# Kernel optimization log

Measured on AMD Instinct MI355X. Metric: run time of the kernel, lower is better.

## Reference

```python
import jax, jax.numpy as jnp
import numpy as np

H = 181  # hidden size

def setup_inputs() -> dict:
    key = jax.random.key(0)
    ks = jax.random.split(key, 7)
    B, T, I, C = 1024, 1024, 1, 10
    x = jax.random.normal(ks[0], (B, T, I), dtype=jnp.float32)
    w_ih = jax.random.normal(ks[1], (3 * H, I), dtype=jnp.float32) * 0.5
    w_hh = jax.random.normal(ks[2], (3 * H, H), dtype=jnp.float32) * (1.0 / np.sqrt(H))
    b_ih = jax.random.normal(ks[3], (3 * H,), dtype=jnp.float32) * 0.1
    b_hh = jax.random.normal(ks[4], (3 * H,), dtype=jnp.float32) * 0.1
    w_fc = jax.random.normal(ks[5], (C, H), dtype=jnp.float32) * (1.0 / np.sqrt(H))
    b_fc = jax.random.normal(ks[6], (C,), dtype=jnp.float32) * 0.1
    return {"x": x, "w_ih": w_ih, "w_hh": w_hh, "b_ih": b_ih, "b_hh": b_hh,
            "w_fc": w_fc, "b_fc": b_fc}

def _gru_last_hidden(x, w_ih, w_hh, b_ih, b_hh):
    # x: [B, T, I]. Precompute input-side gate pre-activations for all steps.
    B = x.shape[0]
    gi = jnp.einsum('bti,gi->btg', x, w_ih) + b_ih  # [B, T, 3H]
    gi = jnp.swapaxes(gi, 0, 1)                     # [T, B, 3H] for scan
    h0 = jnp.zeros((B, H), dtype=x.dtype)

    def step(h, gi_t):
        gh = h @ w_hh.T + b_hh                      # [B, 3H]
        r = jax.nn.sigmoid(gi_t[:, :H] + gh[:, :H])
        z = jax.nn.sigmoid(gi_t[:, H:2 * H] + gh[:, H:2 * H])
        n = jnp.tanh(gi_t[:, 2 * H:] + r * gh[:, 2 * H:])
        h_new = (1.0 - z) * n + z * h
        return h_new, None

    h_last, _ = jax.lax.scan(step, h0, gi)
    return h_last  # [B, H]

def reference(x, w_ih, w_hh, b_ih, b_hh, w_fc, b_fc):
    h_last = _gru_last_hidden(x, w_ih, w_hh, b_ih, b_hh)
    logits = h_last @ w_fc.T + b_fc  # [B, num_classes]
    return logits
```

## Files before the change

### kernel.cpp

```cpp
#include <hip/hip_runtime.h>

#define H 181
#define T_LEN 1024
#define BB 4
#define NBLK 256
#define NTHR 768
#define KT3 3
#define FRAGB 1024
#define PST 192
#define XSTR 1027

typedef __attribute__((ext_vector_type(4))) int intx4;

#define LOG2E 1.4426950408889634f
#define SCH_C  1064992506.0f
#define SCH_LO 897220352.0f
#define SCH_HI 1182433024.0f

__device__ __forceinline__ float exp2_fast(float g) {
    float s = fmaf(g, 8388608.0f, SCH_C);
    s = fminf(fmaxf(s, SCH_LO), SCH_HI);
    return __uint_as_float((unsigned)s);
}
__device__ __forceinline__ float rcpf(float x)   { return __builtin_amdgcn_rcpf(x); }
__device__ __forceinline__ float exp2hw(float x) { return __builtin_amdgcn_exp2f(x); }

__device__ __forceinline__ float row_scale(const float* wrow, bool mv) {
    float rm = 0.0f;
    if (mv) for (int k = 0; k < H; ++k) rm = fmaxf(rm, fabsf(wrow[k]));
    return (rm > 1e-30f) ? rm * (1.0f / 127.0f) : 1.0f;
}

__device__ __forceinline__ intx4 build_frag(const float* wrow, float invs,
                                            bool mv, int kt, int q) {
    intx4 frag;
    #pragma unroll
    for (int w = 0; w < 4; ++w) {
        int dw = 0;
        #pragma unroll
        for (int e = 0; e < 4; ++e) {
            int k = kt * 64 + q * 16 + w * 4 + e;
            float v = (mv && k < H) ? wrow[k] * invs : 0.0f;
            v = fminf(fmaxf(rintf(v), -127.0f), 127.0f);
            int iv = (int)v;
            dw |= (iv & 255) << (8 * e);
        }
        frag[w] = dw;
    }
    return frag;
}

__launch_bounds__(NTHR, 3)
__global__ void gru_i8(const float* __restrict__ x,
                       const float* __restrict__ w_ih,
                       const float* __restrict__ w_hh,
                       const float* __restrict__ b_ih,
                       const float* __restrict__ b_hh,
                       const float* __restrict__ w_fc,
                       const float* __restrict__ b_fc,
                       float* __restrict__ out) {
    __shared__ __align__(16) char  hfr_s[2 * KT3 * FRAGB];
    __shared__ __align__(16) float x_s[BB * XSTR];
    __shared__ float wsc_s[3 * PST];
    __shared__ volatile char pad_s[57344];

    const int tid  = threadIdx.x;
    const int jt   = tid >> 6;
    const int lane = tid & 63;
    const int col  = lane & 15;
    const int q    = lane >> 4;
    const int b0   = blockIdx.x * BB;
    if (tid == 0) pad_s[0] = 0;

    const int  mu = jt * 16 + col;
    const bool mv = (mu < H);
    const float* wrowR = w_hh + (size_t)(0 * H + (mv ? mu : 0)) * H;
    const float* wrowZ = w_hh + (size_t)(1 * H + (mv ? mu : 0)) * H;
    const float* wrowN = w_hh + (size_t)(2 * H + (mv ? mu : 0)) * H;
    const float sR = row_scale(wrowR, mv);
    const float sZ = row_scale(wrowZ, mv);
    const float sN = row_scale(wrowN, mv);
    const float iR = 1.0f / sR, iZ = 1.0f / sZ, iN = 1.0f / sN;
    const intx4 afR0 = build_frag(wrowR, iR, mv, 0, q);
    const intx4 afR1 = build_frag(wrowR, iR, mv, 1, q);
    const intx4 afR2 = build_frag(wrowR, iR, mv, 2, q);
    const intx4 afZ0 = build_frag(wrowZ, iZ, mv, 0, q);
    const intx4 afZ1 = build_frag(wrowZ, iZ, mv, 1, q);
    const intx4 afZ2 = build_frag(wrowZ, iZ, mv, 2, q);
    const intx4 afN0 = build_frag(wrowN, iN, mv, 0, q);
    const intx4 afN1 = build_frag(wrowN, iN, mv, 1, q);
    const intx4 afN2 = build_frag(wrowN, iN, mv, 2, q);
    if (q == 0) {
        wsc_s[0 * PST + mu] = sR;
        wsc_s[1 * PST + mu] = sZ;
        wsc_s[2 * PST + mu] = sN;
    }

    for (int i = tid; i < BB * T_LEN; i += NTHR) {
        int bb = i >> 10, t = i & 1023;
        x_s[bb * XSTR + t] = x[(size_t)b0 * T_LEN + i];
    }
    {
        int* hz = (int*)hfr_s;
        for (int i = tid; i < 2 * KT3 * FRAGB / 4; i += NTHR) hz[i] = 0;
    }
    __syncthreads();

    const int  rr4 = (col >> 2) & 3;
    const int  b   = col & 3;
    const int  u   = jt * 16 + q * 4 + rr4;
    const bool jv  = (u < H);
    const float dqR = -LOG2E * wsc_s[0 * PST + u] * (1.0f / 127.0f);
    const float dqZ = -LOG2E * wsc_s[1 * PST + u] * (1.0f / 127.0f);
    const float dqN =  2.0f * LOG2E * wsc_s[2 * PST + u] * (1.0f / 127.0f);
    const float baseR = jv ? -LOG2E * (b_ih[u] + b_hh[u])             : 0.0f;
    const float baseZ = jv ? -LOG2E * (b_ih[H + u] + b_hh[H + u])     : 0.0f;
    const float baseN = jv ?  2.0f * LOG2E * b_hh[2 * H + u]          : 0.0f;
    const float wrS = jv ? -LOG2E * w_ih[u]                : 0.0f;
    const float wzS = jv ? -LOG2E * w_ih[H + u]            : 0.0f;
    const float wnS = jv ?  2.0f * LOG2E * w_ih[2 * H + u] : 0.0f;
    const float bnI = jv ?  2.0f * LOG2E * b_ih[2 * H + u] : 0.0f;
    const int wboff8 = (jt >> 2) * FRAGB + (((jt & 3) * 16 + b) * 16) + q * 4 + rr4;
    const int rbase = lane * 16;

    float h = 0.0f;

#define STEP(rb, wb, t_) do {                                                 \
    intx4 bf0 = *(const intx4*)((rb) + 0 * FRAGB + rbase);                    \
    intx4 bf1 = *(const intx4*)((rb) + 1 * FRAGB + rbase);                    \
    intx4 bf2 = *(const intx4*)((rb) + 2 * FRAGB + rbase);                    \
    intx4 aR = {0,0,0,0}, aZ = {0,0,0,0}, aN = {0,0,0,0};                     \
    aR = __builtin_amdgcn_mfma_i32_16x16x64_i8(afR0, bf0, aR, 0, 0, 0);       \
    aZ = __builtin_amdgcn_mfma_i32_16x16x64_i8(afZ0, bf0, aZ, 0, 0, 0);       \
    aN = __builtin_amdgcn_mfma_i32_16x16x64_i8(afN0, bf0, aN, 0, 0, 0);       \
    aR = __builtin_amdgcn_mfma_i32_16x16x64_i8(afR1, bf1, aR, 0, 0, 0);       \
    aZ = __builtin_amdgcn_mfma_i32_16x16x64_i8(afZ1, bf1, aZ, 0, 0, 0);       \
    aN = __builtin_amdgcn_mfma_i32_16x16x64_i8(afN1, bf1, aN, 0, 0, 0);       \
    aR = __builtin_amdgcn_mfma_i32_16x16x64_i8(afR2, bf2, aR, 0, 0, 0);       \
    aZ = __builtin_amdgcn_mfma_i32_16x16x64_i8(afZ2, bf2, aZ, 0, 0, 0);       \
    aN = __builtin_amdgcn_mfma_i32_16x16x64_i8(afN2, bf2, aN, 0, 0, 0);       \
    int vR = aR[0], vZ = aZ[0], vN = aN[0];                                   \
    vR = __builtin_amdgcn_update_dpp(vR, aR[1], 0x114, 0xF, 0x2, false);      \
    vR = __builtin_amdgcn_update_dpp(vR, aR[2], 0x118, 0xF, 0x4, false);      \
    vR = __builtin_amdgcn_update_dpp(vR, aR[3], 0x11C, 0xF, 0x8, false);      \
    vZ = __builtin_amdgcn_update_dpp(vZ, aZ[1], 0x114, 0xF, 0x2, false);      \
    vZ = __builtin_amdgcn_update_dpp(vZ, aZ[2], 0x118, 0xF, 0x4, false);      \
    vZ = __builtin_amdgcn_update_dpp(vZ, aZ[3], 0x11C, 0xF, 0x8, false);      \
    vN = __builtin_amdgcn_update_dpp(vN, aN[1], 0x114, 0xF, 0x2, false);      \
    vN = __builtin_amdgcn_update_dpp(vN, aN[2], 0x118, 0xF, 0x4, false);      \
    vN = __builtin_amdgcn_update_dpp(vN, aN[3], 0x11C, 0xF, 0x8, false);      \
    float pR = fmaf((float)vR, dqR, baseR);                                   \
    float pZ = fmaf((float)vZ, dqZ, baseZ);                                   \
    float pN = fmaf((float)vN, dqN, baseN);                                   \
    float xv = x_s[b * XSTR + (t_)];                                          \
    float er = exp2_fast(fmaf(xv, wrS, pR));                                  \
    float ez = exp2hw(fminf(fmaf(xv, wzS, pZ), 14.0f));                       \
    float dR = 1.0f + er, dZ = 1.0f + ez;                                     \
    float qq = rcpf(dR * dZ);                                                 \
    float rr = qq * dZ, zz = qq * dR;                                         \
    float gn = fmaf(rr, pN, fmaf(xv, wnS, bnI));                              \
    float en = exp2hw(fminf(gn, 30.0f));                                      \
    float nn = fmaf(-2.0f, rcpf(1.0f + en), 1.0f);                            \
    h = fmaf(zz, h - nn, nn);                                                 \
    int hq = __float_as_int(fmaf(h, 127.0f, 12582912.0f));                    \
    *(char*)((wb) + wboff8) = (char)hq;                                       \
    __syncthreads();                                                          \
} while (0)

    char* buf0 = hfr_s;
    char* buf1 = hfr_s + KT3 * FRAGB;
    for (int t = 0; t < T_LEN; t += 2) {
        STEP(buf0, buf1, t);
        STEP(buf1, buf0, t + 1);
    }
#undef STEP

    __syncthreads();
    if (u < PST) x_s[b * PST + u] = h;
    __syncthreads();
    if (tid < BB * 10) {
        int bb = tid / 10, c = tid % 10;
        float acc = b_fc[c];
        for (int k = 0; k < H; ++k)
            acc = fmaf(x_s[bb * PST + k], w_fc[c * H + k], acc);
        out[(b0 + bb) * 10 + c] = acc;
    }
}

extern "C" void kernel_launch(void* const* d_in, const int* in_sizes, int n_in,
                              void* d_out, int out_size, void* d_ws, size_t ws_size,
                              hipStream_t stream) {
    const float* x    = (const float*)d_in[0];
    const float* w_ih = (const float*)d_in[1];
    const float* w_hh = (const float*)d_in[2];
    const float* b_ih = (const float*)d_in[3];
    const float* b_hh = (const float*)d_in[4];
    const float* w_fc = (const float*)d_in[5];
    const float* b_fc = (const float*)d_in[6];
    float* out = (float*)d_out;

    gru_i8<<<NBLK, NTHR, 0, stream>>>(x, w_ih, w_hh, b_ih, b_hh, w_fc, b_fc, out);
}
```

Measured before the change: 671.5 us.

## Cut block to 8 waves with first four waves owning two unit tiles

Shrinks each block from 12 to 8 wavefronts: waves 0-3 each handle two 16-unit tiles (A and B) while waves 4-7 handle one, so the 12 tiles of the hidden dimension are still covered. Fewer waves per block means cheaper per-step __syncthreads barriers and less scheduling overhead. In exchange, the critical path for the doubled waves roughly doubles the MFMA and gate work per step, register pressure rises from holding twice the weight fragments, and occupancy drops to two blocks per CU by launch bounds.

```diff
diff --git a/kernel.cpp b/kernel.cpp
--- a/kernel.cpp
+++ b/kernel.cpp
@@ -4,7 +4,7 @@
 #define T_LEN 1024
 #define BB 4
 #define NBLK 256
-#define NTHR 768
+#define NTHR 512
 #define KT3 3
 #define FRAGB 1024
 #define PST 192
@@ -50,7 +50,7 @@
     return frag;
 }
 
-__launch_bounds__(NTHR, 3)
+__launch_bounds__(NTHR, 2)
 __global__ void gru_i8(const float* __restrict__ x,
                        const float* __restrict__ w_ih,
                        const float* __restrict__ w_hh,
@@ -70,30 +70,58 @@
     const int col  = lane & 15;
     const int q    = lane >> 4;
     const int b0   = blockIdx.x * BB;
+    const bool two = (jt < 4);
     if (tid == 0) pad_s[0] = 0;
 
-    const int  mu = jt * 16 + col;
-    const bool mv = (mu < H);
-    const float* wrowR = w_hh + (size_t)(0 * H + (mv ? mu : 0)) * H;
-    const float* wrowZ = w_hh + (size_t)(1 * H + (mv ? mu : 0)) * H;
-    const float* wrowN = w_hh + (size_t)(2 * H + (mv ? mu : 0)) * H;
-    const float sR = row_scale(wrowR, mv);
-    const float sZ = row_scale(wrowZ, mv);
-    const float sN = row_scale(wrowN, mv);
-    const float iR = 1.0f / sR, iZ = 1.0f / sZ, iN = 1.0f / sN;
-    const intx4 afR0 = build_frag(wrowR, iR, mv, 0, q);
-    const intx4 afR1 = build_frag(wrowR, iR, mv, 1, q);
-    const intx4 afR2 = build_frag(wrowR, iR, mv, 2, q);
-    const intx4 afZ0 = build_frag(wrowZ, iZ, mv, 0, q);
-    const intx4 afZ1 = build_frag(wrowZ, iZ, mv, 1, q);
-    const intx4 afZ2 = build_frag(wrowZ, iZ, mv, 2, q);
-    const intx4 afN0 = build_frag(wrowN, iN, mv, 0, q);
-    const intx4 afN1 = build_frag(wrowN, iN, mv, 1, q);
-    const intx4 afN2 = build_frag(wrowN, iN, mv, 2, q);
+    const int  muA = jt * 16 + col;
+    const bool mvA = (muA < H);
+    const float* wrAR = w_hh + (size_t)(0 * H + (mvA ? muA : 0)) * H;
+    const float* wrAZ = w_hh + (size_t)(1 * H + (mvA ? muA : 0)) * H;
+    const float* wrAN = w_hh + (size_t)(2 * H + (mvA ? muA : 0)) * H;
+    const float sAR = row_scale(wrAR, mvA);
+    const float sAZ = row_scale(wrAZ, mvA);
+    const float sAN = row_scale(wrAN, mvA);
+    const intx4 aAR0 = build_frag(wrAR, 1.0f / sAR, mvA, 0, q);
+    const intx4 aAR1 = build_frag(wrAR, 1.0f / sAR, mvA, 1, q);
+    const intx4 aAR2 = build_frag(wrAR, 1.0f / sAR, mvA, 2, q);
+    const intx4 aAZ0 = build_frag(wrAZ, 1.0f / sAZ, mvA, 0, q);
+    const intx4 aAZ1 = build_frag(wrAZ, 1.0f / sAZ, mvA, 1, q);
+    const intx4 aAZ2 = build_frag(wrAZ, 1.0f / sAZ, mvA, 2, q);
+    const intx4 aAN0 = build_frag(wrAN, 1.0f / sAN, mvA, 0, q);
+    const intx4 aAN1 = build_frag(wrAN, 1.0f / sAN, mvA, 1, q);
+    const intx4 aAN2 = build_frag(wrAN, 1.0f / sAN, mvA, 2, q);
     if (q == 0) {
-        wsc_s[0 * PST + mu] = sR;
-        wsc_s[1 * PST + mu] = sZ;
-        wsc_s[2 * PST + mu] = sN;
+        wsc_s[0 * PST + muA] = sAR;
+        wsc_s[1 * PST + muA] = sAZ;
+        wsc_s[2 * PST + muA] = sAN;
+    }
+
+    const int  muB = (8 + jt) * 16 + col;
+    const bool mvB = two && (muB < H);
+    intx4 aBR0 = {0,0,0,0}, aBR1 = {0,0,0,0}, aBR2 = {0,0,0,0};
+    intx4 aBZ0 = {0,0,0,0}, aBZ1 = {0,0,0,0}, aBZ2 = {0,0,0,0};
+    intx4 aBN0 = {0,0,0,0}, aBN1 = {0,0,0,0}, aBN2 = {0,0,0,0};
+    if (two) {
+        const float* wrBR = w_hh + (size_t)(0 * H + (mvB ? muB : 0)) * H;
+        const float* wrBZ = w_hh + (size_t)(1 * H + (mvB ? muB : 0)) * H;
+        const float* wrBN = w_hh + (size_t)(2 * H + (mvB ? muB : 0)) * H;
+        const float sBR = row_scale(wrBR, mvB);
+        const float sBZ = row_scale(wrBZ, mvB);
+        const float sBN = row_scale(wrBN, mvB);
+        aBR0 = build_frag(wrBR, 1.0f / sBR, mvB, 0, q);
+        aBR1 = build_frag(wrBR, 1.0f / sBR, mvB, 1, q);
+        aBR2 = build_frag(wrBR, 1.0f / sBR, mvB, 2, q);
+        aBZ0 = build_frag(wrBZ, 1.0f / sBZ, mvB, 0, q);
+        aBZ1 = build_frag(wrBZ, 1.0f / sBZ, mvB, 1, q);
+        aBZ2 = build_frag(wrBZ, 1.0f / sBZ, mvB, 2, q);
+        aBN0 = build_frag(wrBN, 1.0f / sBN, mvB, 0, q);
+        aBN1 = build_frag(wrBN, 1.0f / sBN, mvB, 1, q);
+        aBN2 = build_frag(wrBN, 1.0f / sBN, mvB, 2, q);
+        if (q == 0) {
+            wsc_s[0 * PST + muB] = sBR;
+            wsc_s[1 * PST + muB] = sBZ;
+            wsc_s[2 * PST + muB] = sBN;
+        }
     }
 
     for (int i = tid; i < BB * T_LEN; i += NTHR) {
@@ -108,62 +136,101 @@
 
     const int  rr4 = (col >> 2) & 3;
     const int  b   = col & 3;
-    const int  u   = jt * 16 + q * 4 + rr4;
-    const bool jv  = (u < H);
-    const float dqR = -LOG2E * wsc_s[0 * PST + u] * (1.0f / 127.0f);
-    const float dqZ = -LOG2E * wsc_s[1 * PST + u] * (1.0f / 127.0f);
-    const float dqN =  2.0f * LOG2E * wsc_s[2 * PST + u] * (1.0f / 127.0f);
-    const float baseR = jv ? -LOG2E * (b_ih[u] + b_hh[u])             : 0.0f;
-    const float baseZ = jv ? -LOG2E * (b_ih[H + u] + b_hh[H + u])     : 0.0f;
-    const float baseN = jv ?  2.0f * LOG2E * b_hh[2 * H + u]          : 0.0f;
-    const float wrS = jv ? -LOG2E * w_ih[u]                : 0.0f;
-    const float wzS = jv ? -LOG2E * w_ih[H + u]            : 0.0f;
-    const float wnS = jv ?  2.0f * LOG2E * w_ih[2 * H + u] : 0.0f;
-    const float bnI = jv ?  2.0f * LOG2E * b_ih[2 * H + u] : 0.0f;
-    const int wboff8 = (jt >> 2) * FRAGB + (((jt & 3) * 16 + b) * 16) + q * 4 + rr4;
+    const int  uA  = jt * 16 + q * 4 + rr4;
+    const int  uB  = (8 + jt) * 16 + q * 4 + rr4;
+    const bool jvA = (uA < H);
+    const bool jvB = two && (uB < H);
+    const float dqRA = -LOG2E * wsc_s[0 * PST + uA] * (1.0f / 127.0f);
+    const float dqZA = -LOG2E * wsc_s[1 * PST + uA] * (1.0f / 127.0f);
+    const float dqNA =  2.0f * LOG2E * wsc_s[2 * PST + uA] * (1.0f / 127.0f);
+    const float baseRA = jvA ? -LOG2E * (b_ih[uA] + b_hh[uA])         : 0.0f;
+    const float baseZA = jvA ? -LOG2E * (b_ih[H + uA] + b_hh[H + uA]) : 0.0f;
+    const float baseNA = jvA ?  2.0f * LOG2E * b_hh[2 * H + uA]       : 0.0f;
+    const float wrSA = jvA ? -LOG2E * w_ih[uA]                : 0.0f;
+    const float wzSA = jvA ? -LOG2E * w_ih[H + uA]            : 0.0f;
+    const float wnSA = jvA ?  2.0f * LOG2E * w_ih[2 * H + uA] : 0.0f;
+    const float bnIA = jvA ?  2.0f * LOG2E * b_ih[2 * H + uA] : 0.0f;
+    const float dqRB = -LOG2E * wsc_s[0 * PST + uB] * (1.0f / 127.0f);
+    const float dqZB = -LOG2E * wsc_s[1 * PST + uB] * (1.0f / 127.0f);
+    const float dqNB =  2.0f * LOG2E * wsc_s[2 * PST + uB] * (1.0f / 127.0f);
+    const float baseRB = jvB ? -LOG2E * (b_ih[uB] + b_hh[uB])         : 0.0f;
+    const float baseZB = jvB ? -LOG2E * (b_ih[H + uB] + b_hh[H + uB]) : 0.0f;
+    const float baseNB = jvB ?  2.0f * LOG2E * b_hh[2 * H + uB]       : 0.0f;
+    const float wrSB = jvB ? -LOG2E * w_ih[uB]                : 0.0f;
+    const float wzSB = jvB ? -LOG2E * w_ih[H + uB]            : 0.0f;
+    const float wnSB = jvB ?  2.0f * LOG2E * w_ih[2 * H + uB] : 0.0f;
+    const float bnIB = jvB ?  2.0f * LOG2E * b_ih[2 * H + uB] : 0.0f;
+    const int woffA = (jt >> 2) * FRAGB + (((jt & 3) * 16 + b) * 16) + q * 4 + rr4;
+    const int woffB = ((8 + jt) >> 2) * FRAGB + ((((8 + jt) & 3) * 16 + b) * 16) + q * 4 + rr4;
     const int rbase = lane * 16;
 
-    float h = 0.0f;
+    float hA = 0.0f, hB = 0.0f;
+
+#define GATES(vR_, vZ_, vN_, dqR_, dqZ_, dqN_, baseR_, baseZ_, baseN_,       \
+              wrS_, wzS_, wnS_, bnI_, h_, wb, woff_) do {                     \
+    float pR = fmaf((float)(vR_), dqR_, baseR_);                              \
+    float pZ = fmaf((float)(vZ_), dqZ_, baseZ_);                              \
+    float pN = fmaf((float)(vN_), dqN_, baseN_);                              \
+    float er = exp2_fast(fmaf(xv, wrS_, pR));                                 \
+    float ez = exp2hw(fminf(fmaf(xv, wzS_, pZ), 14.0f));                      \
+    float dR = 1.0f + er, dZ = 1.0f + ez;                                     \
+    float qq = rcpf(dR * dZ);                                                 \
+    float rr = qq * dZ, zz = qq * dR;                                         \
+    float gn = fmaf(rr, pN, fmaf(xv, wnS_, bnI_));                            \
+    float en = exp2hw(fminf(gn, 30.0f));                                      \
+    float nn = fmaf(-2.0f, rcpf(1.0f + en), 1.0f);                            \
+    h_ = fmaf(zz, h_ - nn, nn);                                               \
+    int hq = __float_as_int(fmaf(h_, 127.0f, 12582912.0f));                   \
+    *(char*)((wb) + (woff_)) = (char)hq;                                      \
+} while (0)
+
+#define DPP3(v_, a_) do {                                                     \
+    v_ = a_[0];                                                               \
+    v_ = __builtin_amdgcn_update_dpp(v_, a_[1], 0x114, 0xF, 0x2, false);      \
+    v_ = __builtin_amdgcn_update_dpp(v_, a_[2], 0x118, 0xF, 0x4, false);      \
+    v_ = __builtin_amdgcn_update_dpp(v_, a_[3], 0x11C, 0xF, 0x8, false);      \
+} while (0)
 
 #define STEP(rb, wb, t_) do {                                                 \
     intx4 bf0 = *(const intx4*)((rb) + 0 * FRAGB + rbase);                    \
     intx4 bf1 = *(const intx4*)((rb) + 1 * FRAGB + rbase);                    \
     intx4 bf2 = *(const intx4*)((rb) + 2 * FRAGB + rbase);                    \
-    intx4 aR = {0,0,0,0}, aZ = {0,0,0,0}, aN = {0,0,0,0};                     \
-    aR = __builtin_amdgcn_mfma_i32_16x16x64_i8(afR0, bf0, aR, 0, 0, 0);       \
-    aZ = __builtin_amdgcn_mfma_i32_16x16x64_i8(afZ0, bf0, aZ, 0, 0, 0);       \
-    aN = __builtin_amdgcn_mfma_i32_16x16x64_i8(afN0, bf0, aN, 0, 0, 0);       \
-    aR = __builtin_amdgcn_mfma_i32_16x16x64_i8(afR1, bf1, aR, 0, 0, 0);       \
-    aZ = __builtin_amdgcn_mfma_i32_16x16x64_i8(afZ1, bf1, aZ, 0, 0, 0);       \
-    aN = __builtin_amdgcn_mfma_i32_16x16x64_i8(afN1, bf1, aN, 0, 0, 0);       \
-    aR = __builtin_amdgcn_mfma_i32_16x16x64_i8(afR2, bf2, aR, 0, 0, 0);       \
-    aZ = __builtin_amdgcn_mfma_i32_16x16x64_i8(afZ2, bf2, aZ, 0, 0, 0);       \
-    aN = __builtin_amdgcn_mfma_i32_16x16x64_i8(afN2, bf2, aN, 0, 0, 0);       \
-    int vR = aR[0], vZ = aZ[0], vN = aN[0];                                   \
-    vR = __builtin_amdgcn_update_dpp(vR, aR[1], 0x114, 0xF, 0x2, false);      \
-    vR = __builtin_amdgcn_update_dpp(vR, aR[2], 0x118, 0xF, 0x4, false);      \
-    vR = __builtin_amdgcn_update_dpp(vR, aR[3], 0x11C, 0xF, 0x8, false);      \
-    vZ = __builtin_amdgcn_update_dpp(vZ, aZ[1], 0x114, 0xF, 0x2, false);      \
-    vZ = __builtin_amdgcn_update_dpp(vZ, aZ[2], 0x118, 0xF, 0x4, false);      \
-    vZ = __builtin_amdgcn_update_dpp(vZ, aZ[3], 0x11C, 0xF, 0x8, false);      \
-    vN = __builtin_amdgcn_update_dpp(vN, aN[1], 0x114, 0xF, 0x2, false);      \
-    vN = __builtin_amdgcn_update_dpp(vN, aN[2], 0x118, 0xF, 0x4, false);      \
-    vN = __builtin_amdgcn_update_dpp(vN, aN[3], 0x11C, 0xF, 0x8, false);      \
-    float pR = fmaf((float)vR, dqR, baseR);                                   \
-    float pZ = fmaf((float)vZ, dqZ, baseZ);                                   \
-    float pN = fmaf((float)vN, dqN, baseN);                                   \
     float xv = x_s[b * XSTR + (t_)];                                          \
-    float er = exp2_fast(fmaf(xv, wrS, pR));                                  \
-    float ez = exp2hw(fminf(fmaf(xv, wzS, pZ), 14.0f));                       \
-    float dR = 1.0f + er, dZ = 1.0f + ez;                                     \
-    float qq = rcpf(dR * dZ);                                                 \
-    float rr = qq * dZ, zz = qq * dR;                                         \
-    float gn = fmaf(rr, pN, fmaf(xv, wnS, bnI));                              \
-    float en = exp2hw(fminf(gn, 30.0f));                                      \
-    float nn = fmaf(-2.0f, rcpf(1.0f + en), 1.0f);                            \
-    h = fmaf(zz, h - nn, nn);                                                 \
-    int hq = __float_as_int(fmaf(h, 127.0f, 12582912.0f));                    \
-    *(char*)((wb) + wboff8) = (char)hq;                                       \
+    intx4 cR = {0,0,0,0}, cZ = {0,0,0,0}, cN = {0,0,0,0};                     \
+    cR = __builtin_amdgcn_mfma_i32_16x16x64_i8(aAR0, bf0, cR, 0, 0, 0);       \
+    cZ = __builtin_amdgcn_mfma_i32_16x16x64_i8(aAZ0, bf0, cZ, 0, 0, 0);       \
+    cN = __builtin_amdgcn_mfma_i32_16x16x64_i8(aAN0, bf0, cN, 0, 0, 0);       \
+    cR = __builtin_amdgcn_mfma_i32_16x16x64_i8(aAR1, bf1, cR, 0, 0, 0);       \
+    cZ = __builtin_amdgcn_mfma_i32_16x16x64_i8(aAZ1, bf1, cZ, 0, 0, 0);       \
+    cN = __builtin_amdgcn_mfma_i32_16x16x64_i8(aAN1, bf1, cN, 0, 0, 0);       \
+    cR = __builtin_amdgcn_mfma_i32_16x16x64_i8(aAR2, bf2, cR, 0, 0, 0);       \
+    cZ = __builtin_amdgcn_mfma_i32_16x16x64_i8(aAZ2, bf2, cZ, 0, 0, 0);       \
+    cN = __builtin_amdgcn_mfma_i32_16x16x64_i8(aAN2, bf2, cN, 0, 0, 0);       \
+    if (two) {                                                                \
+        intx4 eR = {0,0,0,0}, eZ = {0,0,0,0}, eN = {0,0,0,0};                 \
+        eR = __builtin_amdgcn_mfma_i32_16x16x64_i8(aBR0, bf0, eR, 0, 0, 0);   \
+        eZ = __builtin_amdgcn_mfma_i32_16x16x64_i8(aBZ0, bf0, eZ, 0, 0, 0);   \
+        eN = __builtin_amdgcn_mfma_i32_16x16x64_i8(aBN0, bf0, eN, 0, 0, 0);   \
+        eR = __builtin_amdgcn_mfma_i32_16x16x64_i8(aBR1, bf1, eR, 0, 0, 0);   \
+        eZ = __builtin_amdgcn_mfma_i32_16x16x64_i8(aBZ1, bf1, eZ, 0, 0, 0);   \
+        eN = __builtin_amdgcn_mfma_i32_16x16x64_i8(aBN1, bf1, eN, 0, 0, 0);   \
+        eR = __builtin_amdgcn_mfma_i32_16x16x64_i8(aBR2, bf2, eR, 0, 0, 0);   \
+        eZ = __builtin_amdgcn_mfma_i32_16x16x64_i8(aBZ2, bf2, eZ, 0, 0, 0);   \
+        eN = __builtin_amdgcn_mfma_i32_16x16x64_i8(aBN2, bf2, eN, 0, 0, 0);   \
+        int vRB, vZB, vNB;                                                    \
+        DPP3(vRB, eR); DPP3(vZB, eZ); DPP3(vNB, eN);                          \
+        int vRA, vZA, vNA;                                                    \
+        DPP3(vRA, cR); DPP3(vZA, cZ); DPP3(vNA, cN);                          \
+        GATES(vRA, vZA, vNA, dqRA, dqZA, dqNA, baseRA, baseZA, baseNA,        \
+              wrSA, wzSA, wnSA, bnIA, hA, wb, woffA);                         \
+        GATES(vRB, vZB, vNB, dqRB, dqZB, dqNB, baseRB, baseZB, baseNB,        \
+              wrSB, wzSB, wnSB, bnIB, hB, wb, woffB);                         \
+    } else {                                                                  \
+        int vRA, vZA, vNA;                                                    \
+        DPP3(vRA, cR); DPP3(vZA, cZ); DPP3(vNA, cN);                          \
+        GATES(vRA, vZA, vNA, dqRA, dqZA, dqNA, baseRA, baseZA, baseNA,        \
+              wrSA, wzSA, wnSA, bnIA, hA, wb, woffA);                         \
+    }                                                                         \
     __syncthreads();                                                          \
 } while (0)
 
@@ -174,9 +241,12 @@
         STEP(buf1, buf0, t + 1);
     }
 #undef STEP
+#undef GATES
+#undef DPP3
 
     __syncthreads();
-    if (u < PST) x_s[b * PST + u] = h;
+    x_s[b * PST + uA] = hA;
+    if (two) x_s[b * PST + uB] = hB;
     __syncthreads();
     if (tid < BB * 10) {
         int bb = tid / 10, c = tid % 10;
```

Result: slower. 711.5 us (+5.9%).
